# Kernel tuning notes

Hardware: AMD Instinct MI355X
Metric: run time of the kernel (lower is better)

Reference implementation:

```python
import jax, jax.numpy as jnp
import numpy as np
import math

HEAD_SIZE = 128
N_EMBED = 2048
B, T = 4, 4096
TOP_K_RATIO = 0.1


def setup_inputs() -> dict:
    key = jax.random.key(0)
    k1, k2, k3, k4 = jax.random.split(key, 4)
    index = jax.random.normal(k1, (B, T, N_EMBED), dtype=jnp.float32)
    s = 1.0 / math.sqrt(N_EMBED)
    Wq = jax.random.normal(k2, (N_EMBED, HEAD_SIZE), dtype=jnp.float32) * s
    Wk = jax.random.normal(k3, (N_EMBED, HEAD_SIZE), dtype=jnp.float32) * s
    Wv = jax.random.normal(k4, (N_EMBED, HEAD_SIZE), dtype=jnp.float32) * s
    return {"index": index, "Wq": Wq, "Wk": Wk, "Wv": Wv}


def reference(index, Wq, Wk, Wv):
    # memory = index (self-attention case)
    Bv, Tv, _ = index.shape
    top_k = int(TOP_K_RATIO * Tv)  # 409

    q = index @ Wq  # [B, T, D]
    k = index @ Wk
    v = index @ Wv

    q_norms = jnp.linalg.norm(q, axis=-1)  # [B, T]
    _, top_idx = jax.lax.top_k(q_norms, top_k)  # [B, K]

    idx = top_idx[..., None]  # [B, K, 1]
    q_topk = jnp.take_along_axis(q, idx, axis=1)  # [B, K, D]
    k_topk = jnp.take_along_axis(k, idx, axis=1)
    v_topk = jnp.take_along_axis(v, idx, axis=1)

    w = jnp.einsum('bid,bjd->bij', q_topk, k_topk) / math.sqrt(HEAD_SIZE)
    # eval mode: no causal mask (only applied in training), dropout = identity
    w = jax.nn.softmax(w, axis=-1)  # stable softmax (internal max subtraction)
    out_topk = w @ v_topk  # [B, K, D]

    batch_idx = jnp.arange(Bv)[:, None]  # [B, 1]
    output = jnp.zeros((Bv, Tv, HEAD_SIZE), dtype=out_topk.dtype)
    output = output.at[batch_idx, top_idx].add(out_topk)  # scatter_add (indices unique)
    return output
```

## Files before the change

kernel.cpp:

```cpp
#include <hip/hip_runtime.h>
#include <hip/hip_bf16.h>

#define NB 4
#define NT 4096
#define NC 2048
#define ND 128
#define NK 409
#define KPAD 416
#define NM (NB * NK)

typedef __attribute__((ext_vector_type(8))) short short8;
typedef __attribute__((ext_vector_type(4))) float f32x4;

union S8U { short8 v; ushort u[8]; };

__device__ __forceinline__ void split2(float x, ushort& h, ushort& l) {
    union { float f; unsigned u; } a; a.f = x;
    unsigned r = a.u + 0x7FFFu + ((a.u >> 16) & 1u);
    h = (ushort)(r >> 16);
    union { unsigned u; float f; } hb; hb.u = ((unsigned)h) << 16;
    float res = x - hb.f;
    union { float f; unsigned u; } b; b.f = res;
    unsigned r2 = b.u + 0x7FFFu + ((b.u >> 16) & 1u);
    l = (ushort)(r2 >> 16);
}

__device__ __forceinline__ uint4 pack8(const ushort* s) {
    uint4 v;
    v.x = (unsigned)s[0] | ((unsigned)s[1] << 16);
    v.y = (unsigned)s[2] | ((unsigned)s[3] << 16);
    v.z = (unsigned)s[4] | ((unsigned)s[5] << 16);
    v.w = (unsigned)s[6] | ((unsigned)s[7] << 16);
    return v;
}

__device__ __forceinline__ int slotOf(int n, int lq) {
    return n * 4 + ((lq + (n >> 1)) & 3);
}

__global__ __launch_bounds__(256) void bconv_tiles(
    const float* __restrict__ W, ushort* __restrict__ Bt)
{
    const int kt = blockIdx.x;
    const int t = threadIdx.x;
    const int n = t & 127;
    const int lq0 = (t >> 7) * 2;
    #pragma unroll
    for (int e = 0; e < 2; ++e) {
        int lq = lq0 + e;
        ushort h[8], l[8];
        #pragma unroll
        for (int j = 0; j < 8; ++j) {
            float x = W[(size_t)(kt * 32 + lq * 8 + j) * ND + n];
            split2(x, h[j], l[j]);
        }
        int slot = slotOf(n, lq);
        *(uint4*)&Bt[((size_t)(kt * 2 + 0) * 512 + slot) * 8] = pack8(h);
        *(uint4*)&Bt[((size_t)(kt * 2 + 1) * 512 + slot) * 8] = pack8(l);
    }
}

#define QSTEP(BHC, BLC, BHN, BLN, KTN)                                        \
    {                                                                         \
        short8 ah, al;                                                        \
        {                                                                     \
            S8U H, L;                                                         \
            float xs[8] = {fa0.x, fa0.y, fa0.z, fa0.w,                        \
                           fa1.x, fa1.y, fa1.z, fa1.w};                       \
            _Pragma("unroll")                                                 \
            for (int j = 0; j < 8; ++j) split2(xs[j], H.u[j], L.u[j]);        \
            ah = H.v; al = L.v;                                               \
        }                                                                     \
        const ushort* gbn = Bt + (size_t)(kt0 + (KTN)) * 8192;                \
        _Pragma("unroll")                                                     \
        for (int ni = 0; ni < 8; ++ni) {                                      \
            BHN[ni] = *(const short8*)(gbn + boff[ni]);                       \
            BLN[ni] = *(const short8*)(gbn + 4096 + boff[ni]);                \
        }                                                                     \
        fa0 = *(const float4*)(arow + (KTN) * 32);                            \
        fa1 = *(const float4*)(arow + (KTN) * 32 + 4);                        \
        _Pragma("unroll")                                                     \
        for (int ni = 0; ni < 8; ++ni) {                                      \
            acc[ni] = __builtin_amdgcn_mfma_f32_16x16x32_bf16(ah, BHC[ni], acc[ni], 0, 0, 0); \
            acc[ni] = __builtin_amdgcn_mfma_f32_16x16x32_bf16(ah, BLC[ni], acc[ni], 0, 0, 0); \
            acc[ni] = __builtin_amdgcn_mfma_f32_16x16x32_bf16(al, BHC[ni], acc[ni], 0, 0, 0); \
        }                                                                     \
    }

#define QSPLIT 2
__global__ __launch_bounds__(256) void qgemm_v8(
    const float* __restrict__ A, const ushort* __restrict__ Bt,
    float* __restrict__ q1, float* __restrict__ q2)
{
    const int tid = threadIdx.x;
    const int w = tid >> 6, lane = tid & 63;
    const int lrow = lane & 15, lq = lane >> 4;
    const int m0 = blockIdx.x * 64;
    const int KITER = (NC / QSPLIT) / 32;
    const int kt0 = blockIdx.y * KITER;
    const int kb = blockIdx.y * (NC / QSPLIT);
    const int phase = blockIdx.x & (KITER - 1);

    const float* arow = A + (size_t)(m0 + w * 16 + lrow) * NC + kb + lq * 8;

    int boff[8];
    #pragma unroll
    for (int ni = 0; ni < 8; ++ni)
        boff[ni] = slotOf(ni * 16 + lrow, lq) * 8;

    f32x4 acc[8];
    #pragma unroll
    for (int i = 0; i < 8; ++i) acc[i] = (f32x4){0.f, 0.f, 0.f, 0.f};

    short8 bhA[8], blA[8], bhB[8], blB[8];
    {
        const ushort* gb = Bt + (size_t)(kt0 + phase) * 8192;
        #pragma unroll
        for (int ni = 0; ni < 8; ++ni) {
            bhA[ni] = *(const short8*)(gb + boff[ni]);
            blA[ni] = *(const short8*)(gb + 4096 + boff[ni]);
        }
    }
    float4 fa0 = *(const float4*)(arow + phase * 32);
    float4 fa1 = *(const float4*)(arow + phase * 32 + 4);

    int ktc = phase;
    for (int it = 0; it < KITER; it += 2) {
        QSTEP(bhA, blA, bhB, blB, ((ktc + 1) & (KITER - 1)));
        QSTEP(bhB, blB, bhA, blA, ((ktc + 2) & (KITER - 1)));
        ktc = (ktc + 2) & (KITER - 1);
    }

    float* __restrict__ qd = blockIdx.y ? q2 : q1;
    #pragma unroll
    for (int ni = 0; ni < 8; ++ni) {
        const int col = ni * 16 + lrow;
        #pragma unroll
        for (int r = 0; r < 4; ++r) {
            const int grow = m0 + w * 16 + lq * 4 + r;
            qd[(size_t)grow * ND + col] = acc[ni][r];
        }
    }
}

#define KVSPLIT 8
__global__ __launch_bounds__(256) void kvgemm_v8(
    const float* __restrict__ X, const ushort* __restrict__ Bkt,
    const ushort* __restrict__ Bvt, const int* __restrict__ topi,
    float* __restrict__ ktop, float* __restrict__ vtop)
{
    const int tid = threadIdx.x;
    const int w = tid >> 6, lane = tid & 63;
    const int lrow = lane & 15, lq = lane >> 4;
    const int m0 = blockIdx.x * 64;
    const int KITER = (NC / KVSPLIT) / 32;
    const int kt0 = blockIdx.y * KITER;
    const int kb = blockIdx.y * (NC / KVSPLIT);
    const ushort* __restrict__ Bt = blockIdx.z ? Bvt : Bkt;
    const int phase = (blockIdx.x * 3 + blockIdx.y) & (KITER - 1);

    const int gi = m0 + w * 16 + lrow;
    const int giC = gi < NM ? gi : NM - 1;
    const int b = giC / NK, ii = giC % NK;
    const int src = topi[b * KPAD + ii];
    const float* arow = X + ((size_t)b * NT + src) * NC + kb + lq * 8;

    int boff[8];
    #pragma unroll
    for (int ni = 0; ni < 8; ++ni)
        boff[ni] = slotOf(ni * 16 + lrow, lq) * 8;

    f32x4 acc[8];
    #pragma unroll
    for (int i = 0; i < 8; ++i) acc[i] = (f32x4){0.f, 0.f, 0.f, 0.f};

    short8 bhA[8], blA[8], bhB[8], blB[8];
    {
        const ushort* gb = Bt + (size_t)(kt0 + phase) * 8192;
        #pragma unroll
        for (int ni = 0; ni < 8; ++ni) {
            bhA[ni] = *(const short8*)(gb + boff[ni]);
            blA[ni] = *(const short8*)(gb + 4096 + boff[ni]);
        }
    }
    float4 fa0 = *(const float4*)(arow + phase * 32);
    float4 fa1 = *(const float4*)(arow + phase * 32 + 4);

    int ktc = phase;
    for (int it = 0; it < KITER; it += 2) {
        QSTEP(bhA, blA, bhB, blB, ((ktc + 1) & (KITER - 1)));
        QSTEP(bhB, blB, bhA, blA, ((ktc + 2) & (KITER - 1)));
        ktc = (ktc + 2) & (KITER - 1);
    }

    float* __restrict__ dst = blockIdx.z ? vtop : ktop;
    #pragma unroll
    for (int ni = 0; ni < 8; ++ni) {
        const int col = ni * 16 + lrow;
        #pragma unroll
        for (int r = 0; r < 4; ++r) {
            const int grow = m0 + w * 16 + lq * 4 + r;
            if (grow < NM)
                atomicAdd(&dst[(size_t)grow * ND + col], acc[ni][r]);
        }
    }
}

__global__ __launch_bounds__(256) void qnorm_kernel(
    float* __restrict__ q1, const float* __restrict__ q2, float* __restrict__ qn)
{
    const int wv = (blockIdx.x * 256 + threadIdx.x) >> 6;
    const int lane = threadIdx.x & 63;
    float* r1 = q1 + (size_t)wv * ND;
    const float* r2 = q2 + (size_t)wv * ND;
    float a = r1[lane] + r2[lane];
    float b = r1[lane + 64] + r2[lane + 64];
    r1[lane] = a;
    r1[lane + 64] = b;
    float s = a * a + b * b;
    #pragma unroll
    for (int off = 32; off > 0; off >>= 1) s += __shfl_xor(s, off);
    if (lane == 0) qn[wv] = sqrtf(s);
}

__global__ __launch_bounds__(256) void topk_kernel(
    const float* __restrict__ qn, int* __restrict__ topi, int* __restrict__ cnt)
{
    __shared__ int rs[4][64];
    const int b = blockIdx.y;
    const int is = threadIdx.x & 63;
    const int i = blockIdx.x * 64 + is;
    const int chunk = threadIdx.x >> 6;
    const float vi = qn[(size_t)b * NT + i];
    const float4* qv = (const float4*)(qn + (size_t)b * NT + chunk * 1024);
    int rank = 0;
    #pragma unroll 4
    for (int j4 = 0; j4 < 256; ++j4) {
        float4 v = qv[j4];
        int j = chunk * 1024 + j4 * 4;
        rank += (v.x > vi || (v.x == vi && (j + 0) < i)) ? 1 : 0;
        rank += (v.y > vi || (v.y == vi && (j + 1) < i)) ? 1 : 0;
        rank += (v.z > vi || (v.z == vi && (j + 2) < i)) ? 1 : 0;
        rank += (v.w > vi || (v.w == vi && (j + 3) < i)) ? 1 : 0;
    }
    rs[chunk][is] = rank;
    __syncthreads();
    if (threadIdx.x < 64) {
        int rk = rs[0][threadIdx.x] + rs[1][threadIdx.x] + rs[2][threadIdx.x] + rs[3][threadIdx.x];
        if (rk < NK) {
            int p = atomicAdd(&cnt[b], 1);
            topi[b * KPAD + p] = blockIdx.x * 64 + threadIdx.x;
        }
    }
}

__global__ __launch_bounds__(256) void attn_kernel(
    const float* __restrict__ q, const float* __restrict__ ktop,
    const float* __restrict__ vtop, const int* __restrict__ topi,
    float* __restrict__ out)
{
    __shared__ float qs[ND];
    __shared__ float ss[KPAD];
    __shared__ float red[256];
    __shared__ float pv[2][ND];
    const int bi = blockIdx.x;
    const int b = bi / NK, i = bi % NK;
    const int t = threadIdx.x;
    const int row = topi[b * KPAD + i];
    if (t < ND) qs[t] = q[((size_t)b * NT + row) * ND + t];
    __syncthreads();

    const float scale = 0.08838834764831844f;
    float mymax = -1e30f;
    #pragma unroll
    for (int rep = 0; rep < 2; ++rep) {
        int j = t + rep * 256;
        if (j < NK) {
            const float4* kr = (const float4*)(ktop + ((size_t)b * NK + j) * ND);
            const float4* q4 = (const float4*)qs;
            float s = 0.f;
            #pragma unroll
            for (int dd = 0; dd < 32; ++dd) {
                float4 a = q4[dd], kv = kr[dd];
                s += a.x * kv.x + a.y * kv.y + a.z * kv.z + a.w * kv.w;
            }
            s *= scale;
            ss[j] = s;
            mymax = fmaxf(mymax, s);
        }
    }
    red[t] = mymax;
    __syncthreads();
    for (int off = 128; off > 0; off >>= 1) {
        if (t < off) red[t] = fmaxf(red[t], red[t + off]);
        __syncthreads();
    }
    const float mx = red[0];
    __syncthreads();

    float mysum = 0.f;
    #pragma unroll
    for (int rep = 0; rep < 2; ++rep) {
        int j = t + rep * 256;
        if (j < NK) {
            float p = __expf(ss[j] - mx);
            ss[j] = p;
            mysum += p;
        }
    }
    red[t] = mysum;
    __syncthreads();
    for (int off = 128; off > 0; off >>= 1) {
        if (t < off) red[t] += red[t + off];
        __syncthreads();
    }
    const float inv = 1.f / red[0];

    const int col = t & (ND - 1), half = t >> 7;
    float o = 0.f;
    #pragma unroll 4
    for (int j = half; j < NK; j += 2)
        o = fmaf(ss[j], vtop[((size_t)b * NK + j) * ND + col], o);
    pv[half][col] = o;
    __syncthreads();
    if (t < ND)
        out[((size_t)b * NT + row) * ND + t] = (pv[0][t] + pv[1][t]) * inv;
}

extern "C" void kernel_launch(void* const* d_in, const int* in_sizes, int n_in,
                              void* d_out, int out_size, void* d_ws, size_t ws_size,
                              hipStream_t stream)
{
    const float* index = (const float*)d_in[0];
    const float* Wq = (const float*)d_in[1];
    const float* Wk = (const float*)d_in[2];
    const float* Wv = (const float*)d_in[3];
    float* out = (float*)d_out;

    char* ws = (char*)d_ws;
    float*  q1   = (float*)(ws);
    float*  qn   = (float*)(ws + 8388608);
    int*    topi = (int*)  (ws + 8454144);
    int*    cnt  = (int*)  (ws + 8462336);
    ushort* Bqt  = (ushort*)(ws + 8462592);
    float*  ktop = (float*)(ws + 8462592);
    float*  vtop = (float*)(ws + 9300224);

    float*  q2  = (float*)d_out;
    ushort* Bkt = (ushort*)d_out;
    ushort* Bvt = (ushort*)((char*)d_out + 1048576);

    hipMemsetAsync(cnt, 0, NB * sizeof(int), stream);

    bconv_tiles<<<dim3(64), dim3(256), 0, stream>>>(Wq, Bqt);
    qgemm_v8<<<dim3(NB * NT / 64, QSPLIT), dim3(256), 0, stream>>>(index, Bqt, q1, q2);
    qnorm_kernel<<<dim3(NB * NT / 4), dim3(256), 0, stream>>>(q1, q2, qn);
    topk_kernel<<<dim3(NT / 64, NB), dim3(256), 0, stream>>>(qn, topi, cnt);
    bconv_tiles<<<dim3(64), dim3(256), 0, stream>>>(Wk, Bkt);
    bconv_tiles<<<dim3(64), dim3(256), 0, stream>>>(Wv, Bvt);
    hipMemsetAsync(ktop, 0, 2 * 837632, stream);
    kvgemm_v8<<<dim3((NM + 63) / 64, KVSPLIT, 2), dim3(256), 0, stream>>>(
        index, Bkt, Bvt, topi, ktop, vtop);
    hipMemsetAsync(d_out, 0, (size_t)out_size * sizeof(float), stream);
    attn_kernel<<<dim3(NM), dim3(256), 0, stream>>>(q1, ktop, vtop, topi, out);
}
```

Baseline: 381.1 us.

## Prefetch A operand in four-step bursts and drop per-block k-phase rotation

```diff
diff --git a/kernel.cpp b/kernel.cpp
--- a/kernel.cpp
+++ b/kernel.cpp
@@ -60,13 +60,13 @@
     }
 }
 
-#define QSTEP(BHC, BLC, BHN, BLN, KTN)                                        \
+#define QSTEP(BHC, BLC, BHN, BLN, KTN, F0, F1)                                \
     {                                                                         \
         short8 ah, al;                                                        \
         {                                                                     \
             S8U H, L;                                                         \
-            float xs[8] = {fa0.x, fa0.y, fa0.z, fa0.w,                        \
-                           fa1.x, fa1.y, fa1.z, fa1.w};                       \
+            float xs[8] = {F0.x, F0.y, F0.z, F0.w,                            \
+                           F1.x, F1.y, F1.z, F1.w};                           \
             _Pragma("unroll")                                                 \
             for (int j = 0; j < 8; ++j) split2(xs[j], H.u[j], L.u[j]);        \
             ah = H.v; al = L.v;                                               \
@@ -77,8 +77,6 @@
             BHN[ni] = *(const short8*)(gbn + boff[ni]);                       \
             BLN[ni] = *(const short8*)(gbn + 4096 + boff[ni]);                \
         }                                                                     \
-        fa0 = *(const float4*)(arow + (KTN) * 32);                            \
-        fa1 = *(const float4*)(arow + (KTN) * 32 + 4);                        \
         _Pragma("unroll")                                                     \
         for (int ni = 0; ni < 8; ++ni) {                                      \
             acc[ni] = __builtin_amdgcn_mfma_f32_16x16x32_bf16(ah, BHC[ni], acc[ni], 0, 0, 0); \
@@ -87,8 +85,15 @@
         }                                                                     \
     }
 
+#define ABURST(FB, KT4)                                                       \
+    _Pragma("unroll")                                                         \
+    for (int s = 0; s < 4; ++s) {                                             \
+        FB[s][0] = *(const float4*)(arow + ((KT4) + s) * 32);                 \
+        FB[s][1] = *(const float4*)(arow + ((KT4) + s) * 32 + 4);             \
+    }
+
 #define QSPLIT 2
-__global__ __launch_bounds__(256) void qgemm_v8(
+__global__ __launch_bounds__(256) void qgemm_v10(
     const float* __restrict__ A, const ushort* __restrict__ Bt,
     float* __restrict__ q1, float* __restrict__ q2)
 {
@@ -99,7 +104,6 @@
     const int KITER = (NC / QSPLIT) / 32;
     const int kt0 = blockIdx.y * KITER;
     const int kb = blockIdx.y * (NC / QSPLIT);
-    const int phase = blockIdx.x & (KITER - 1);
 
     const float* arow = A + (size_t)(m0 + w * 16 + lrow) * NC + kb + lq * 8;
 
@@ -114,21 +118,28 @@
 
     short8 bhA[8], blA[8], bhB[8], blB[8];
     {
-        const ushort* gb = Bt + (size_t)(kt0 + phase) * 8192;
+        const ushort* gb = Bt + (size_t)kt0 * 8192;
         #pragma unroll
         for (int ni = 0; ni < 8; ++ni) {
             bhA[ni] = *(const short8*)(gb + boff[ni]);
             blA[ni] = *(const short8*)(gb + 4096 + boff[ni]);
         }
     }
-    float4 fa0 = *(const float4*)(arow + phase * 32);
-    float4 fa1 = *(const float4*)(arow + phase * 32 + 4);
-
-    int ktc = phase;
-    for (int it = 0; it < KITER; it += 2) {
-        QSTEP(bhA, blA, bhB, blB, ((ktc + 1) & (KITER - 1)));
-        QSTEP(bhB, blB, bhA, blA, ((ktc + 2) & (KITER - 1)));
-        ktc = (ktc + 2) & (KITER - 1);
+    float4 faA[4][2], faB[4][2];
+    ABURST(faA, 0);
+
+    for (int g = 0; g < 8; g += 2) {
+        ABURST(faB, g * 4 + 4);
+        QSTEP(bhA, blA, bhB, blB, g * 4 + 1, faA[0][0], faA[0][1]);
+        QSTEP(bhB, blB, bhA, blA, g * 4 + 2, faA[1][0], faA[1][1]);
+        QSTEP(bhA, blA, bhB, blB, g * 4 + 3, faA[2][0], faA[2][1]);
+        QSTEP(bhB, blB, bhA, blA, g * 4 + 4, faA[3][0], faA[3][1]);
+        if (g + 2 < 8) { ABURST(faA, g * 4 + 8); }
+        QSTEP(bhA, blA, bhB, blB, g * 4 + 5, faB[0][0], faB[0][1]);
+        QSTEP(bhB, blB, bhA, blA, g * 4 + 6, faB[1][0], faB[1][1]);
+        QSTEP(bhA, blA, bhB, blB, g * 4 + 7, faB[2][0], faB[2][1]);
+        QSTEP(bhB, blB, bhA, blA, (g * 4 + 8 < 32 ? g * 4 + 8 : 31),
+              faB[3][0], faB[3][1]);
     }
 
     float* __restrict__ qd = blockIdx.y ? q2 : q1;
@@ -144,7 +155,7 @@
 }
 
 #define KVSPLIT 8
-__global__ __launch_bounds__(256) void kvgemm_v8(
+__global__ __launch_bounds__(256) void kvgemm_v10(
     const float* __restrict__ X, const ushort* __restrict__ Bkt,
     const ushort* __restrict__ Bvt, const int* __restrict__ topi,
     float* __restrict__ ktop, float* __restrict__ vtop)
@@ -157,7 +168,6 @@
     const int kt0 = blockIdx.y * KITER;
     const int kb = blockIdx.y * (NC / KVSPLIT);
     const ushort* __restrict__ Bt = blockIdx.z ? Bvt : Bkt;
-    const int phase = (blockIdx.x * 3 + blockIdx.y) & (KITER - 1);
 
     const int gi = m0 + w * 16 + lrow;
     const int giC = gi < NM ? gi : NM - 1;
@@ -176,22 +186,25 @@
 
     short8 bhA[8], blA[8], bhB[8], blB[8];
     {
-        const ushort* gb = Bt + (size_t)(kt0 + phase) * 8192;
+        const ushort* gb = Bt + (size_t)kt0 * 8192;
         #pragma unroll
         for (int ni = 0; ni < 8; ++ni) {
             bhA[ni] = *(const short8*)(gb + boff[ni]);
             blA[ni] = *(const short8*)(gb + 4096 + boff[ni]);
         }
     }
-    float4 fa0 = *(const float4*)(arow + phase * 32);
-    float4 fa1 = *(const float4*)(arow + phase * 32 + 4);
-
-    int ktc = phase;
-    for (int it = 0; it < KITER; it += 2) {
-        QSTEP(bhA, blA, bhB, blB, ((ktc + 1) & (KITER - 1)));
-        QSTEP(bhB, blB, bhA, blA, ((ktc + 2) & (KITER - 1)));
-        ktc = (ktc + 2) & (KITER - 1);
-    }
+    float4 faA[4][2], faB[4][2];
+    ABURST(faA, 0);
+    ABURST(faB, 4);
+
+    QSTEP(bhA, blA, bhB, blB, 1, faA[0][0], faA[0][1]);
+    QSTEP(bhB, blB, bhA, blA, 2, faA[1][0], faA[1][1]);
+    QSTEP(bhA, blA, bhB, blB, 3, faA[2][0], faA[2][1]);
+    QSTEP(bhB, blB, bhA, blA, 4, faA[3][0], faA[3][1]);
+    QSTEP(bhA, blA, bhB, blB, 5, faB[0][0], faB[0][1]);
+    QSTEP(bhB, blB, bhA, blA, 6, faB[1][0], faB[1][1]);
+    QSTEP(bhA, blA, bhB, blB, 7, faB[2][0], faB[2][1]);
+    QSTEP(bhB, blB, bhA, blA, 7, faB[3][0], faB[3][1]);
 
     float* __restrict__ dst = blockIdx.z ? vtop : ktop;
     #pragma unroll
@@ -353,13 +366,13 @@
     hipMemsetAsync(cnt, 0, NB * sizeof(int), stream);
 
     bconv_tiles<<<dim3(64), dim3(256), 0, stream>>>(Wq, Bqt);
-    qgemm_v8<<<dim3(NB * NT / 64, QSPLIT), dim3(256), 0, stream>>>(index, Bqt, q1, q2);
+    qgemm_v10<<<dim3(NB * NT / 64, QSPLIT), dim3(256), 0, stream>>>(index, Bqt, q1, q2);
     qnorm_kernel<<<dim3(NB * NT / 4), dim3(256), 0, stream>>>(q1, q2, qn);
     topk_kernel<<<dim3(NT / 64, NB), dim3(256), 0, stream>>>(qn, topi, cnt);
     bconv_tiles<<<dim3(64), dim3(256), 0, stream>>>(Wk, Bkt);
     bconv_tiles<<<dim3(64), dim3(256), 0, stream>>>(Wv, Bvt);
     hipMemsetAsync(ktop, 0, 2 * 837632, stream);
-    kvgemm_v8<<<dim3((NM + 63) / 64, KVSPLIT, 2), dim3(256), 0, stream>>>(
+    kvgemm_v10<<<dim3((NM + 63) / 64, KVSPLIT, 2), dim3(256), 0, stream>>>(
         index, Bkt, Bvt, topi, ktop, vtop);
     hipMemsetAsync(d_out, 0, (size_t)out_size * sizeof(float), stream);
     attn_kernel<<<dim3(NM), dim3(256), 0, stream>>>(q1, ktop, vtop, topi, out);
```

New measurement: 377.3 us. About the same (-1.0%).
